# Optimization experiments

Hardware: AMD Instinct MI355X
Metric: run time of the kernel (lower is better)

The kernel has to match this reference:

```python
import jax, jax.numpy as jnp
import numpy as np

D_MODEL = 768
N_HEADS = 12

def setup_inputs() -> dict:
    key = jax.random.key(0)
    ks = jax.random.split(key, 5)
    D = D_MODEL
    x = jax.random.normal(ks[0], (2, 4096, D), dtype=jnp.float32)
    s_attn = 1.0 / np.sqrt(D)
    s_proj = 1.0 / np.sqrt(D)
    W_attn = jax.random.uniform(ks[1], (D, 3 * D), minval=-s_attn, maxval=s_attn, dtype=jnp.float32)
    b_attn = jax.random.uniform(ks[2], (3 * D,), minval=-s_attn, maxval=s_attn, dtype=jnp.float32)
    W_proj = jax.random.uniform(ks[3], (D, D), minval=-s_proj, maxval=s_proj, dtype=jnp.float32)
    b_proj = jax.random.uniform(ks[4], (D,), minval=-s_proj, maxval=s_proj, dtype=jnp.float32)
    return {"x": x, "W_attn": W_attn, "b_attn": b_attn, "W_proj": W_proj, "b_proj": b_proj}

def reference(x, W_attn, b_attn, W_proj, b_proj):
    B, T, C = x.shape
    H = N_HEADS
    hd = C // H
    qkv = x @ W_attn + b_attn                     # [B,T,3C]
    q, k, v = jnp.split(qkv, 3, axis=-1)
    # [B,T,C] -> [B,H,T,hd]
    q = q.reshape(B, T, H, hd).transpose(0, 2, 1, 3)
    k = k.reshape(B, T, H, hd).transpose(0, 2, 1, 3)
    v = v.reshape(B, T, H, hd).transpose(0, 2, 1, 3)
    att = jnp.einsum('bhqd,bhkd->bhqk', q, k) * (1.0 / np.sqrt(hd))
    causal = jnp.tril(jnp.ones((T, T), dtype=bool))
    att = jnp.where(causal, att, -jnp.inf)
    att = jax.nn.softmax(att, axis=-1)
    y = jnp.einsum('bhqk,bhkd->bhqd', att, v)     # [B,H,T,hd]
    y = y.transpose(0, 2, 1, 3).reshape(B, T, C)
    return y @ W_proj + b_proj
```

## Files before the change

### kernel.cpp

```cpp
#include <hip/hip_runtime.h>
#include <hip/hip_bf16.h>

typedef __attribute__((ext_vector_type(8))) short bf16x8;
typedef __attribute__((ext_vector_type(4))) float f32x4;
typedef __attribute__((ext_vector_type(16))) float f32x16;
typedef __attribute__((ext_vector_type(4))) int i32x4;

#define DEVI __device__ __forceinline__

namespace {
constexpr int BATCH = 2;
constexpr int T = 4096;
constexpr int C = 768;
constexpr int H = 12;
constexpr int HD = 64;
constexpr int M = BATCH * T;
constexpr int N3 = 3 * C;
constexpr int BH = BATCH * H;
constexpr float QSCALE = 0.125f * 1.44269504088896f;
constexpr float SMAX = 32.0f;
constexpr int PSZ = 64 * 128 + 128;
}

DEVI ushort f2b(float f) {
  union { float f; unsigned u; } v; v.f = f;
  unsigned r = (v.u + 0x7FFFu + ((v.u >> 16) & 1u)) >> 16;
  return (ushort)r;
}

DEVI f32x16 zero16() {
  f32x16 z;
#pragma unroll
  for (int i = 0; i < 16; i++) z[i] = 0.f;
  return z;
}

DEVI void gload16(const void* g, void* l) {
  __builtin_amdgcn_global_load_lds(
      (const __attribute__((address_space(1))) unsigned int*)g,
      (__attribute__((address_space(3))) unsigned int*)l, 16, 0, 0);
}

__global__ __launch_bounds__(256) void cvt_kernel(const float* __restrict__ src,
                                                  ushort* __restrict__ dst, int n) {
  int i = (blockIdx.x * 256 + threadIdx.x) * 4;
  int stride = gridDim.x * 256 * 4;
  for (; i < n; i += stride) {
    float4 v = *reinterpret_cast<const float4*>(src + i);
    ushort4 o;
    o.x = f2b(v.x); o.y = f2b(v.y); o.z = f2b(v.z); o.w = f2b(v.w);
    *reinterpret_cast<ushort4*>(dst + i) = o;
  }
}

__global__ __launch_bounds__(256) void cvtT_kernel(const float* __restrict__ src,
                                                   ushort* __restrict__ dst,
                                                   int K, int N) {
  __shared__ ushort Lt[64 * 68];
  const int k0 = blockIdx.x * 64, n0 = blockIdx.y * 64;
  const int tid = threadIdx.x;
  const int rr = tid >> 4, c4 = (tid & 15) * 4;
#pragma unroll
  for (int it = 0; it < 4; it++) {
    const int r = it * 16 + rr;
    float4 v = *reinterpret_cast<const float4*>(src + (size_t)(k0 + r) * N + n0 + c4);
    Lt[(c4 + 0) * 68 + r] = f2b(v.x);
    Lt[(c4 + 1) * 68 + r] = f2b(v.y);
    Lt[(c4 + 2) * 68 + r] = f2b(v.z);
    Lt[(c4 + 3) * 68 + r] = f2b(v.w);
  }
  __syncthreads();
#pragma unroll
  for (int it = 0; it < 4; it++) {
    const int r = it * 16 + rr;
    *reinterpret_cast<ushort4*>(dst + (size_t)(n0 + r) * K + k0 + c4) =
        *reinterpret_cast<const ushort4*>(&Lt[r * 68 + c4]);
  }
}

template <int EPI>
__global__ __launch_bounds__(256, 3) void gemm_kernel(
    const ushort* __restrict__ A, const ushort* __restrict__ Bt,
    const float* __restrict__ bias, int N, int Kd,
    ushort* __restrict__ qo, ushort* __restrict__ ko, ushort* __restrict__ vo,
    float* __restrict__ fo) {
  constexpr int BM = (EPI == 0) ? 128 : 64;
  constexpr int BN = 128;
  constexpr int WN = (EPI == 0) ? 2 : 4;
  constexpr int WTN = BN / WN;
  constexpr int NT = WTN / 32;
  constexpr int CH_A = BM / 8;
  constexpr int CH_B = BN / 8;
  constexpr int CPW = (CH_A + CH_B) / 4;
  constexpr int SMEM = (EPI == 0) ? (4 * 64 * 68) : ((BM + BN) * 64);
  __shared__ ushort smem[SMEM];
  ushort* As = smem;
  ushort* Bs = smem + BM * 64;

  const int tid = threadIdx.x;
  const int lane = tid & 63;
  const int w = tid >> 6;
  const int l31 = lane & 31;
  const int hi = lane >> 5;
  const int wm = w / WN, wn = w % WN;
  const int m0 = blockIdx.y * BM, n0 = blockIdx.x * BN;
  const int r8 = lane >> 3, c8 = lane & 7;
  const int csw = (c8 ^ r8) * 8;

  f32x16 acc[2][NT];
#pragma unroll
  for (int mt = 0; mt < 2; mt++)
#pragma unroll
    for (int nt = 0; nt < NT; nt++) acc[mt][nt] = zero16();

  for (int k0 = 0; k0 < Kd; k0 += 64) {
    __syncthreads();
#pragma unroll
    for (int ci = 0; ci < CPW; ci++) {
      const int chk = w * CPW + ci;
      if (chk < CH_A) {
        gload16(A + (size_t)(m0 + chk * 8 + r8) * Kd + k0 + csw, (char*)As + chk * 1024);
      } else {
        const int ch2 = chk - CH_A;
        gload16(Bt + (size_t)(n0 + ch2 * 8 + r8) * Kd + k0 + csw, (char*)Bs + ch2 * 1024);
      }
    }
    __syncthreads();
#pragma unroll
    for (int ks = 0; ks < 4; ks++) {
      bf16x8 af[2], bf[NT];
#pragma unroll
      for (int mt = 0; mt < 2; mt++) {
        const int rl = wm * 64 + mt * 32 + l31;
        af[mt] = *reinterpret_cast<const bf16x8*>(
            &As[rl * 64 + ((ks * 16 + hi * 8) ^ ((rl & 7) * 8))]);
      }
#pragma unroll
      for (int nt = 0; nt < NT; nt++) {
        const int nl = wn * WTN + nt * 32 + l31;
        bf[nt] = *reinterpret_cast<const bf16x8*>(
            &Bs[nl * 64 + ((ks * 16 + hi * 8) ^ ((nl & 7) * 8))]);
      }
#pragma unroll
      for (int mt = 0; mt < 2; mt++)
#pragma unroll
        for (int nt = 0; nt < NT; nt++)
          acc[mt][nt] = __builtin_amdgcn_mfma_f32_32x32x16_bf16(af[mt], bf[nt], acc[mt][nt], 0, 0, 0);
    }
  }

  if constexpr (EPI == 0) {
    if (n0 >= 1536) {
      __syncthreads();
      ushort* Vw = smem + w * 4352;
      const float bv0 = bias[n0 + wn * 64 + l31];
      const float bv1 = bias[n0 + wn * 64 + 32 + l31];
#pragma unroll
      for (int mt = 0; mt < 2; mt++)
#pragma unroll
        for (int nt = 0; nt < 2; nt++) {
          const float bv = nt ? bv1 : bv0;
#pragma unroll
          for (int r = 0; r < 16; r++) {
            const int trow = mt * 32 + (r & 3) + ((r >> 2) << 3) + (hi << 2);
            Vw[(nt * 32 + l31) * 68 + trow] = f2b(acc[mt][nt][r] + bv);
          }
        }
      const int hh = (n0 - 1536) / 64 + wn;
      const int bb = m0 >> 12;
      const int t0 = (m0 & (T - 1)) + wm * 64;
      const size_t vbase = (size_t)((bb * H + hh) * 64 + lane) * T + t0;
#pragma unroll
      for (int x8 = 0; x8 < 8; x8++) {
        bf16x8 vv = *reinterpret_cast<const bf16x8*>(&Vw[lane * 68 + x8 * 8]);
        *reinterpret_cast<bf16x8*>(vo + vbase + ((x8 ^ (lane & 7)) * 8)) = vv;
      }
    } else {
#pragma unroll
      for (int mt = 0; mt < 2; mt++)
#pragma unroll
        for (int nt = 0; nt < 2; nt++) {
          const int n = n0 + wn * 64 + nt * 32 + l31;
          const float bv = bias[n];
          const int part = (n >= 768) ? 1 : 0;
          const int ci = n - part * 768;
          const int hh = ci >> 6, dd = ci & 63;
#pragma unroll
          for (int r = 0; r < 16; r++) {
            const int m = m0 + wm * 64 + mt * 32 + (r & 3) + ((r >> 2) << 3) + (hi << 2);
            const int bb = m >> 12, t = m & (T - 1);
            const float val = acc[mt][nt][r] + bv;
            if (part == 0) {
              qo[((size_t)(bb * H + hh) * T + t) * HD + dd] = f2b(val * QSCALE);
            } else {
              ko[((size_t)(bb * H + hh) * T + t) * HD + (dd ^ ((t & 7) << 3))] = f2b(val);
            }
          }
        }
    }
  } else {
#pragma unroll
    for (int mt = 0; mt < 2; mt++)
#pragma unroll
      for (int nt = 0; nt < NT; nt++) {
        const int n = n0 + wn * WTN + nt * 32 + l31;
        const float bv = bias[n];
#pragma unroll
        for (int r = 0; r < 16; r++) {
          const int m = m0 + wm * 64 + mt * 32 + (r & 3) + ((r >> 2) << 3) + (hi << 2);
          fo[(size_t)m * N + n] = acc[mt][nt][r] + bv;
        }
      }
  }
}

__global__ __launch_bounds__(256, 3) void attn_kernel(
    const ushort* __restrict__ Qg, const ushort* __restrict__ Kg,
    const ushort* __restrict__ Vtg, ushort* __restrict__ Yg,
    float* __restrict__ Pp) {
  __shared__ ushort kbuf[128 * 64];
  __shared__ ushort vbuf[2 * 2 * 64 * 64];

  const int tid = threadIdx.x;
  const int lane = tid & 63;
  const int w = tid >> 6;
  const int l31 = lane & 31;
  const int hi = lane >> 5;
  const int r8 = lane >> 3, c8 = lane & 7;

  const int bid = blockIdx.x;
  const int xcd = bid & 7, idx = bid >> 3;
  const int bh = xcd * 3 + idx % 3;
  const int slot = idx / 3;

  int qtA, qtB, kvbase, bnd, ntot, pA, pB;
  if (slot < 8) {
    qtA = slot; qtB = 15 - slot; kvbase = 0; bnd = slot + 1; ntot = 17; pA = -1; pB = -1;
  } else if (slot < 24) {
    qtA = slot + 8; qtB = -1; kvbase = 0; bnd = 100; ntot = 16;
    pA = (bh * 16 + (qtA - 16)) * 2; pB = -1;
  } else {
    const int a = slot - 24;
    qtA = 16 + a; qtB = 31 - a; kvbase = 16; bnd = a + 1; ntot = 17;
    pA = (bh * 16 + a) * 2 + 1; pB = (bh * 16 + (15 - a)) * 2 + 1;
  }

  const int bb = bh / H, h = bh % H;
  const ushort* Qp = Qg + (size_t)bh * T * HD;
  const char* Kbp = (const char*)(Kg + (size_t)bh * T * HD);
  const char* Vbp = (const char*)(Vtg + (size_t)bh * HD * T);

  bf16x8 qcur[4];
#pragma unroll
  for (int ks = 0; ks < 4; ks++)
    qcur[ks] = *reinterpret_cast<const bf16x8*>(
        Qp + (size_t)(qtA * 128 + w * 32 + l31) * HD + ks * 16 + hi * 8);

  int qtcur = qtA;
  int q0 = qtA * 128, q0w = q0 + w * 32, qc = q0w + l31;
  int pcur = pA;

  f32x16 o16[2];
  o16[0] = zero16();
  o16[1] = zero16();
  float sa = 0.f, sb = 0.f, sc = 0.f, sd = 0.f;
  const int swz = (l31 & 7) << 3;

  auto issue_K = [&](int kvt) {
    const int kv0 = kvt * 128;
#pragma unroll
    for (int c2 = 0; c2 < 4; c2++) {
      const int chk = w * 4 + c2;
      gload16(Kbp + ((size_t)(kv0 + chk * 8 + r8) * 64 + c8 * 8) * 2,
              (char*)kbuf + chk * 1024);
    }
  };
  auto issue_V = [&](int kvt, int par) {
    const int kv0 = kvt * 128;
#pragma unroll
    for (int c2 = 0; c2 < 4; c2++) {
      const int chk = w * 4 + c2;
      const int st = chk >> 3;
      const int d8 = chk & 7;
      gload16(Vbp + ((size_t)(d8 * 8 + r8) * T + kv0 + st * 64 + c8 * 8) * 2,
              (char*)vbuf + par * 16384 + chk * 1024);
    }
  };

  auto epilogue = [&](int q0p, float lr, ushort* Ytb) {
    ushort* Yw = Ytb + w * 1152;
    const float linv = 1.0f / lr;
#pragma unroll
    for (int dt = 0; dt < 2; dt++) {
#pragma unroll
      for (int r = 0; r < 16; r++) {
        const int d32 = (r & 3) + ((r >> 2) << 3) + (hi << 2);
        Yw[l31 * 36 + d32] = f2b(o16[dt][r] * linv);
      }
#pragma unroll
      for (int seg = 0; seg < 2; seg++) {
        bf16x8 vv = *reinterpret_cast<const bf16x8*>(&Yw[l31 * 36 + hi * 16 + seg * 8]);
        *reinterpret_cast<bf16x8*>(
            Yg + ((size_t)(bb * T + q0p + w * 32 + l31)) * C + h * 64 + dt * 32 +
            hi * 16 + seg * 8) = vv;
      }
    }
  };

  auto pwrite = [&](float* P, float lr) {
#pragma unroll
    for (int dt = 0; dt < 2; dt++)
#pragma unroll
      for (int r = 0; r < 16; r++) {
        const int d = dt * 32 + (r & 3) + ((r >> 2) << 3) + (hi << 2);
        P[d * 128 + w * 32 + l31] = o16[dt][r];
      }
    P[8192 + w * 32 + l31] = lr;
  };

  issue_K(kvbase);
  issue_V(kvbase, 0);

  for (int tt = 0; tt < ntot; tt++) {
    asm volatile("s_waitcnt vmcnt(0)" ::: "memory");
    __builtin_amdgcn_s_barrier();
    __builtin_amdgcn_sched_barrier(0);

    if (tt == bnd) {
      float lr = (sa + sb) + (sc + sd);
      lr += __shfl_xor(lr, 32);
      if (pcur >= 0) pwrite(Pp + (size_t)pcur * PSZ, lr);
      else epilogue(q0, lr, vbuf + ((tt + 1) & 1) * 8192);
      o16[0] = zero16(); o16[1] = zero16();
      sa = sb = sc = sd = 0.f;
#pragma unroll
      for (int ks = 0; ks < 4; ks++)
        qcur[ks] = *reinterpret_cast<const bf16x8*>(
            Qp + (size_t)(qtB * 128 + w * 32 + l31) * HD + ks * 16 + hi * 8);
      qtcur = qtB; q0 = qtB * 128; q0w = q0 + w * 32; qc = q0w + l31; pcur = pB;
    }

    const int kvt = kvbase + (tt < bnd ? tt : tt - bnd);
    const int kv0 = kvt * 128;
    bool have[4], needm[4];
#pragma unroll
    for (int sub = 0; sub < 4; sub++) {
      have[sub] = (kv0 + sub * 32) <= (q0w + 31);
      needm[sub] = (kv0 + sub * 32 + 31) > q0w;
    }

    f32x16 s2[4];
#pragma unroll
    for (int sub = 0; sub < 4; sub++) {
      if (!have[sub]) continue;
      f32x16 acc = zero16();
      const int row = sub * 32 + l31;
      __builtin_amdgcn_s_setprio(1);
#pragma unroll
      for (int ks = 0; ks < 4; ks++) {
        bf16x8 kf = *reinterpret_cast<const bf16x8*>(
            &kbuf[row * 64 + ((ks * 16 + hi * 8) ^ swz)]);
        acc = __builtin_amdgcn_mfma_f32_32x32x16_bf16(kf, qcur[ks], acc, 0, 0, 0);
      }
      __builtin_amdgcn_s_setprio(0);
      if (needm[sub]) {
#pragma unroll
        for (int r2 = 0; r2 < 16; r2++) {
          const int kv = kv0 + sub * 32 + (r2 & 3) + ((r2 >> 2) << 3) + (hi << 2);
          if (kv > qc) acc[r2] = -1e30f;
        }
      }
      s2[sub] = acc;
    }

    asm volatile("s_waitcnt lgkmcnt(0)" ::: "memory");
    __builtin_amdgcn_s_barrier();
    __builtin_amdgcn_sched_barrier(0);
    if (tt + 1 < ntot) {
      const int nkvt = kvbase + ((tt + 1) < bnd ? (tt + 1) : (tt + 1) - bnd);
      issue_K(nkvt);
      issue_V(nkvt, (tt + 1) & 1);
    }

#pragma unroll
    for (int sub = 0; sub < 4; sub++) {
      if (!have[sub]) continue;
#pragma unroll
      for (int r2 = 0; r2 < 16; r2 += 4) {
        s2[sub][r2]     = __builtin_amdgcn_exp2f(s2[sub][r2] - SMAX);     sa += s2[sub][r2];
        s2[sub][r2 + 1] = __builtin_amdgcn_exp2f(s2[sub][r2 + 1] - SMAX); sb += s2[sub][r2 + 1];
        s2[sub][r2 + 2] = __builtin_amdgcn_exp2f(s2[sub][r2 + 2] - SMAX); sc += s2[sub][r2 + 2];
        s2[sub][r2 + 3] = __builtin_amdgcn_exp2f(s2[sub][r2 + 3] - SMAX); sd += s2[sub][r2 + 3];
      }
    }

    const ushort* Vpar = vbuf + (tt & 1) * 8192;
#pragma unroll
    for (int sub = 0; sub < 4; sub++) {
      if (!have[sub]) continue;
      const ushort* Vst = Vpar + (sub >> 1) * 4096;
      const int colb = (sub & 1) * 32;
#pragma unroll
      for (int ks2 = 0; ks2 < 2; ks2++) {
        const int r0 = ks2 * 8;
        int a0, a1, b0, b1;
        asm("v_cvt_pk_bf16_f32 %0, %1, %2" : "=v"(a0) : "v"(s2[sub][r0 + 0]), "v"(s2[sub][r0 + 1]));
        asm("v_cvt_pk_bf16_f32 %0, %1, %2" : "=v"(a1) : "v"(s2[sub][r0 + 2]), "v"(s2[sub][r0 + 3]));
        asm("v_cvt_pk_bf16_f32 %0, %1, %2" : "=v"(b0) : "v"(s2[sub][r0 + 4]), "v"(s2[sub][r0 + 5]));
        asm("v_cvt_pk_bf16_f32 %0, %1, %2" : "=v"(b1) : "v"(s2[sub][r0 + 6]), "v"(s2[sub][r0 + 7]));
        asm("v_permlane32_swap_b32 %0, %1" : "+v"(a0), "+v"(b0));
        asm("v_permlane32_swap_b32 %0, %1" : "+v"(a1), "+v"(b1));
        const i32x4 pi = {a0, a1, b0, b1};
        const bf16x8 pf = __builtin_bit_cast(bf16x8, pi);
        __builtin_amdgcn_s_setprio(1);
#pragma unroll
        for (int dt = 0; dt < 2; dt++) {
          const int drow = dt * 32 + l31;
          const int sw2 = (drow & 7) << 3;
          bf16x8 vf = *reinterpret_cast<const bf16x8*>(
              &Vst[drow * 64 + ((colb + ks2 * 16 + hi * 8) ^ sw2)]);
          o16[dt] = __builtin_amdgcn_mfma_f32_32x32x16_bf16(vf, pf, o16[dt], 0, 0, 0);
        }
        __builtin_amdgcn_s_setprio(0);
      }
    }
  }

  {
    float lr = (sa + sb) + (sc + sd);
    lr += __shfl_xor(lr, 32);
    if (pcur >= 0) pwrite(Pp + (size_t)pcur * PSZ, lr);
    else epilogue(q0, lr, vbuf + (ntot & 1) * 8192);
  }
}

__global__ __launch_bounds__(128) void combine_kernel(const float* __restrict__ Pp,
                                                      ushort* __restrict__ Yg) {
  __shared__ ushort Yt[128 * 68];
  const int bid = blockIdx.x;
  const int bh = bid >> 4, qq = bid & 15;
  const int bb = bh / H, h = bh % H;
  const int q0 = (16 + qq) * 128;
  const int q = threadIdx.x;
  const float* P1 = Pp + (size_t)(bh * 16 + qq) * 2 * PSZ;
  const float* P2 = P1 + PSZ;
  const float inv = 1.0f / (P1[8192 + q] + P2[8192 + q]);
#pragma unroll 8
  for (int d = 0; d < 64; d++)
    Yt[q * 68 + d] = f2b((P1[d * 128 + q] + P2[d * 128 + q]) * inv);
  __syncthreads();
#pragma unroll
  for (int it = 0; it < 2; it++) {
    const int row = it * 64 + (q >> 1), half = q & 1;
#pragma unroll
    for (int seg = 0; seg < 4; seg++) {
      bf16x8 vv = *reinterpret_cast<const bf16x8*>(&Yt[row * 68 + half * 32 + seg * 8]);
      *reinterpret_cast<bf16x8*>(
          Yg + ((size_t)(bb * T + q0 + row)) * C + h * 64 + half * 32 + seg * 8) = vv;
    }
  }
}

extern "C" void kernel_launch(void* const* d_in, const int* in_sizes, int n_in,
                              void* d_out, int out_size, void* d_ws, size_t ws_size,
                              hipStream_t stream) {
  const float* x = (const float*)d_in[0];
  const float* Wa = (const float*)d_in[1];
  const float* ba = (const float*)d_in[2];
  const float* Wp = (const float*)d_in[3];
  const float* bp = (const float*)d_in[4];
  float* out = (float*)d_out;

  char* ws = (char*)d_ws;
  size_t off = 0;
  auto carve = [&](size_t bytes) {
    void* p = ws + off;
    off += (bytes + 255) & ~(size_t)255;
    return p;
  };
  ushort* xb   = (ushort*)carve((size_t)M * C * 2);
  ushort* WaT  = (ushort*)carve((size_t)N3 * C * 2);
  ushort* WpT  = (ushort*)carve((size_t)C * C * 2);
  ushort* Qb   = (ushort*)carve((size_t)BH * T * HD * 2);
  ushort* Kb   = (ushort*)carve((size_t)BH * T * HD * 2);
  ushort* Vtb  = (ushort*)carve((size_t)BH * HD * T * 2);
  ushort* Yb   = (ushort*)carve((size_t)M * C * 2);
  float*  Pp   = (float*)carve((size_t)BH * 16 * 2 * PSZ * 4);

  cvt_kernel<<<2048, 256, 0, stream>>>(x, xb, M * C);
  cvtT_kernel<<<dim3(C / 64, N3 / 64), 256, 0, stream>>>(Wa, WaT, C, N3);
  cvtT_kernel<<<dim3(C / 64, C / 64), 256, 0, stream>>>(Wp, WpT, C, C);

  gemm_kernel<0><<<dim3(N3 / 128, M / 128), 256, 0, stream>>>(
      xb, WaT, ba, N3, C, Qb, Kb, Vtb, nullptr);

  attn_kernel<<<dim3(768), 256, 0, stream>>>(Qb, Kb, Vtb, Yb, Pp);
  combine_kernel<<<dim3(BH * 16), 128, 0, stream>>>(Pp, Yb);

  gemm_kernel<1><<<dim3(C / 128, M / 64), 256, 0, stream>>>(
      Yb, WpT, bp, C, C, nullptr, nullptr, nullptr, out);
}
```

Before: 169.6 us.

## Compute softmax row sums via MFMA with ones, drop SMAX shift, enlarge proj tiles

The attention kernel no longer accumulates the softmax denominator with scalar adds and a cross-lane shuffle. It feeds the bf16 probabilities through an extra MFMA against a vector of ones, so the row sum comes out of the matrix unit. The constant SMAX shift before exp2 is removed, which relies on the scores staying small enough not to overflow, and the first QK MFMA now takes a zero accumulator directly. The output-projection GEMM also switches to 128x128 tiles with the same warp layout as the QKV GEMM, halving its grid size.

```diff
diff --git a/kernel.cpp b/kernel.cpp
--- a/kernel.cpp
+++ b/kernel.cpp
@@ -18,7 +18,6 @@
 constexpr int N3 = 3 * C;
 constexpr int BH = BATCH * H;
 constexpr float QSCALE = 0.125f * 1.44269504088896f;
-constexpr float SMAX = 32.0f;
 constexpr int PSZ = 64 * 128 + 128;
 }
 
@@ -84,9 +83,9 @@
     const float* __restrict__ bias, int N, int Kd,
     ushort* __restrict__ qo, ushort* __restrict__ ko, ushort* __restrict__ vo,
     float* __restrict__ fo) {
-  constexpr int BM = (EPI == 0) ? 128 : 64;
+  constexpr int BM = 128;
   constexpr int BN = 128;
-  constexpr int WN = (EPI == 0) ? 2 : 4;
+  constexpr int WN = 2;
   constexpr int WTN = BN / WN;
   constexpr int NT = WTN / 32;
   constexpr int CH_A = BM / 8;
@@ -256,14 +255,17 @@
     qcur[ks] = *reinterpret_cast<const bf16x8*>(
         Qp + (size_t)(qtA * 128 + w * 32 + l31) * HD + ks * 16 + hi * 8);
 
-  int qtcur = qtA;
   int q0 = qtA * 128, q0w = q0 + w * 32, qc = q0w + l31;
   int pcur = pA;
+
+  const f32x16 ZF = zero16();
+  const i32x4 onesi = {0x3F803F80, 0x3F803F80, 0x3F803F80, 0x3F803F80};
+  const bf16x8 onesf = __builtin_bit_cast(bf16x8, onesi);
 
   f32x16 o16[2];
   o16[0] = zero16();
   o16[1] = zero16();
-  float sa = 0.f, sb = 0.f, sc = 0.f, sd = 0.f;
+  f32x16 o_l = zero16();
   const int swz = (l31 & 7) << 3;
 
   auto issue_K = [&](int kvt) {
@@ -327,17 +329,15 @@
     __builtin_amdgcn_sched_barrier(0);
 
     if (tt == bnd) {
-      float lr = (sa + sb) + (sc + sd);
-      lr += __shfl_xor(lr, 32);
+      const float lr = o_l[0];
       if (pcur >= 0) pwrite(Pp + (size_t)pcur * PSZ, lr);
       else epilogue(q0, lr, vbuf + ((tt + 1) & 1) * 8192);
-      o16[0] = zero16(); o16[1] = zero16();
-      sa = sb = sc = sd = 0.f;
+      o16[0] = zero16(); o16[1] = zero16(); o_l = zero16();
 #pragma unroll
       for (int ks = 0; ks < 4; ks++)
         qcur[ks] = *reinterpret_cast<const bf16x8*>(
             Qp + (size_t)(qtB * 128 + w * 32 + l31) * HD + ks * 16 + hi * 8);
-      qtcur = qtB; q0 = qtB * 128; q0w = q0 + w * 32; qc = q0w + l31; pcur = pB;
+      q0 = qtB * 128; q0w = q0 + w * 32; qc = q0w + l31; pcur = pB;
     }
 
     const int kvt = kvbase + (tt < bnd ? tt : tt - bnd);
@@ -353,12 +353,13 @@
 #pragma unroll
     for (int sub = 0; sub < 4; sub++) {
       if (!have[sub]) continue;
-      f32x16 acc = zero16();
       const int row = sub * 32 + l31;
       __builtin_amdgcn_s_setprio(1);
-#pragma unroll
-      for (int ks = 0; ks < 4; ks++) {
-        bf16x8 kf = *reinterpret_cast<const bf16x8*>(
+      bf16x8 kf = *reinterpret_cast<const bf16x8*>(&kbuf[row * 64 + ((hi * 8) ^ swz)]);
+      f32x16 acc = __builtin_amdgcn_mfma_f32_32x32x16_bf16(kf, qcur[0], ZF, 0, 0, 0);
+#pragma unroll
+      for (int ks = 1; ks < 4; ks++) {
+        kf = *reinterpret_cast<const bf16x8*>(
             &kbuf[row * 64 + ((ks * 16 + hi * 8) ^ swz)]);
         acc = __builtin_amdgcn_mfma_f32_32x32x16_bf16(kf, qcur[ks], acc, 0, 0, 0);
       }
@@ -386,12 +387,8 @@
     for (int sub = 0; sub < 4; sub++) {
       if (!have[sub]) continue;
 #pragma unroll
-      for (int r2 = 0; r2 < 16; r2 += 4) {
-        s2[sub][r2]     = __builtin_amdgcn_exp2f(s2[sub][r2] - SMAX);     sa += s2[sub][r2];
-        s2[sub][r2 + 1] = __builtin_amdgcn_exp2f(s2[sub][r2 + 1] - SMAX); sb += s2[sub][r2 + 1];
-        s2[sub][r2 + 2] = __builtin_amdgcn_exp2f(s2[sub][r2 + 2] - SMAX); sc += s2[sub][r2 + 2];
-        s2[sub][r2 + 3] = __builtin_amdgcn_exp2f(s2[sub][r2 + 3] - SMAX); sd += s2[sub][r2 + 3];
-      }
+      for (int r2 = 0; r2 < 16; r2++)
+        s2[sub][r2] = __builtin_amdgcn_exp2f(s2[sub][r2]);
     }
 
     const ushort* Vpar = vbuf + (tt & 1) * 8192;
@@ -421,14 +418,14 @@
               &Vst[drow * 64 + ((colb + ks2 * 16 + hi * 8) ^ sw2)]);
           o16[dt] = __builtin_amdgcn_mfma_f32_32x32x16_bf16(vf, pf, o16[dt], 0, 0, 0);
         }
+        o_l = __builtin_amdgcn_mfma_f32_32x32x16_bf16(onesf, pf, o_l, 0, 0, 0);
         __builtin_amdgcn_s_setprio(0);
       }
     }
   }
 
   {
-    float lr = (sa + sb) + (sc + sd);
-    lr += __shfl_xor(lr, 32);
+    const float lr = o_l[0];
     if (pcur >= 0) pwrite(Pp + (size_t)pcur * PSZ, lr);
     else epilogue(q0, lr, vbuf + (ntot & 1) * 8192);
   }
@@ -497,6 +494,6 @@
   attn_kernel<<<dim3(768), 256, 0, stream>>>(Qb, Kb, Vtb, Yb, Pp);
   combine_kernel<<<dim3(BH * 16), 128, 0, stream>>>(Pp, Yb);
 
-  gemm_kernel<1><<<dim3(C / 128, M / 64), 256, 0, stream>>>(
+  gemm_kernel<1><<<dim3(C / 128, M / 128), 256, 0, stream>>>(
       Yb, WpT, bp, C, C, nullptr, nullptr, nullptr, out);
 }
```

Result: slower. 189.0 us (+11.4%).
